# Performance work log

Hardware: AMD Instinct MI355X
Metric: run time of the kernel (lower is better)

## Reference

```python
import jax, jax.numpy as jnp
import numpy as np

D_MODEL = 256
N_HEADS = 8
HEAD_DIM = D_MODEL // N_HEADS


def setup_inputs() -> dict:
    key = jax.random.key(0)
    ks = jax.random.split(key, 10)
    B, L, D = 2, 2048, D_MODEL
    s = 1.0 / np.sqrt(D)
    inp = {
        "x": jax.random.normal(ks[0], (B, L, D), dtype=jnp.float32),
        "Wq": jax.random.normal(ks[1], (D, D), dtype=jnp.float32) * s,
        "bq": jnp.zeros((D,), jnp.float32),
        "Wk": jax.random.normal(ks[2], (D, D), dtype=jnp.float32) * s,
        "bk": jnp.zeros((D,), jnp.float32),
        "Wv": jax.random.normal(ks[3], (D, D), dtype=jnp.float32) * s,
        "bv": jnp.zeros((D,), jnp.float32),
        "u": jax.random.normal(ks[4], (N_HEADS, 1, 1), dtype=jnp.float32) * 0.1,
        "Wo": jax.random.normal(ks[5], (D, D), dtype=jnp.float32) * s,
        "bo": jnp.zeros((D,), jnp.float32),
    }
    return inp


def reference(x, Wq, bq, Wk, bk, Wv, bv, u, Wo, bo):
    B, L, D = x.shape
    H, hd = N_HEADS, HEAD_DIM

    def proj(W, b):  # torch Linear: x @ W.T + b -> [B,H,L,hd]
        return (x @ W.T + b).reshape(B, L, H, hd).transpose(0, 2, 1, 3)

    Q, K, V = proj(Wq, bq), proj(Wk, bk), proj(Wv, bv)

    scores = jnp.einsum("bhqd,bhkd->bhqk", Q, K) / np.sqrt(hd)
    attn_series = jax.nn.softmax(scores, axis=-1)  # [B,H,L,L]

    pos = jnp.arange(L, dtype=jnp.float32)
    dist = jnp.abs(pos[None, :] - pos[:, None])  # [L,L]
    # prior per head: exp(-d^2 / (2*(u^2+1e-6))), normalized over last dim
    prior = jnp.exp(-(dist[None] ** 2) / (2.0 * (u ** 2 + 1e-6)))  # [H,L,L]
    prior = prior / (prior.sum(axis=-1, keepdims=True) + 1e-6)

    discrepancy = jnp.abs(attn_series - prior[None]).mean(axis=(1, 2))  # [B,L]

    out = jnp.einsum("bhqk,bhkd->bhqd", attn_series, V)
    out = out.transpose(0, 2, 1, 3).reshape(B, L, D)
    out = out @ Wo.T + bo
    return out, discrepancy
```

## Files before the change

kernel.cpp:

```cpp
#include <hip/hip_runtime.h>
#include <hip/hip_bf16.h>
#include <math.h>

#define LSEQ 2048
#define DMODEL 256
#define NH 8
#define HD 32

typedef __attribute__((ext_vector_type(8))) short bf16x8;
typedef __attribute__((ext_vector_type(4))) float f32x4;

#define MFMA __builtin_amdgcn_mfma_f32_16x16x32_bf16

__device__ __forceinline__ short f2bf(float x) {
  __hip_bfloat16 h = __float2bfloat16(x);
  return __builtin_bit_cast(short, h);
}
__device__ __forceinline__ float bf2f(short s) {
  __hip_bfloat16 h = __builtin_bit_cast(__hip_bfloat16, s);
  return __bfloat162float(h);
}
__device__ __forceinline__ short bftrunc(float x) {
  return (short)(__builtin_bit_cast(unsigned int, x) >> 16);
}
__device__ __forceinline__ float fexp2(float x) {
#if __has_builtin(__builtin_amdgcn_exp2f)
  return __builtin_amdgcn_exp2f(x);
#else
  return __expf(x * 0.6931471805599453f);
#endif
}
__device__ __forceinline__ float flog2(float x) {
#if __has_builtin(__builtin_amdgcn_logf)
  return __builtin_amdgcn_logf(x);
#else
  return __logf(x) * 1.4426950408889634f;
#endif
}

__global__ __launch_bounds__(256) void aux_kernel(
    const float* __restrict__ Wq, const float* __restrict__ Wk,
    const float* __restrict__ Wv, const float* __restrict__ Wo,
    const float* __restrict__ u,
    short* __restrict__ Wh,
    short* __restrict__ Woh, short* __restrict__ Wol,
    float* __restrict__ Eb, float* __restrict__ Zb)
{
  __shared__ float Cs[LSEQ];
  __shared__ float part[256];
  const int tid = threadIdx.x;
  if (blockIdx.x < 256) {
    const int i4 = (blockIdx.x * 256 + tid) * 4;
    if (i4 < 196608) {
      int row = i4 >> 8, col = i4 & 255;
      const float* W = (row < 256) ? Wq : (row < 512) ? Wk : Wv;
      float4 v = *(const float4*)(W + (row & 255) * 256 + col);
      *(short4*)(Wh + i4) = make_short4(f2bf(v.x), f2bf(v.y), f2bf(v.z), f2bf(v.w));
    } else {
      int j = i4 - 196608;
      float4 v = *(const float4*)(Wo + j);
      short h0 = f2bf(v.x), h1 = f2bf(v.y), h2 = f2bf(v.z), h3 = f2bf(v.w);
      *(short4*)(Woh + j) = make_short4(h0, h1, h2, h3);
      *(short4*)(Wol + j) = make_short4(bftrunc(v.x - bf2f(h0)), bftrunc(v.y - bf2f(h1)),
                                        bftrunc(v.z - bf2f(h2)), bftrunc(v.w - bf2f(h3)));
    }
    return;
  }
  const int h = blockIdx.x - 256;
  const float uu = u[h];
  const float den = 2.0f * (uu * uu + 1e-6f);
  float e[8]; float run = 0.f;
  const int base = tid * 8;
#pragma unroll
  for (int j = 0; j < 8; ++j) {
    float d = (float)(base + j);
    e[j] = __expf(-(d * d) / den);
    run += e[j];
  }
  part[tid] = run;
  __syncthreads();
  for (int off = 1; off < 256; off <<= 1) {
    float v = (tid >= off) ? part[tid - off] : 0.f;
    __syncthreads();
    part[tid] += v;
    __syncthreads();
  }
  float c = part[tid] - run;
#pragma unroll
  for (int j = 0; j < 8; ++j) {
    c += e[j];
    Cs[base + j] = c;
    Eb[h * LSEQ + base + j] = e[j];
  }
  __syncthreads();
  const float E0 = Cs[0];
  for (int i = tid; i < LSEQ; i += 256) {
    float s = Cs[i] + Cs[LSEQ - 1 - i] - E0;
    Zb[h * LSEQ + i] = 1.0f / (s + 1e-6f);
  }
}

__global__ __launch_bounds__(256) void qkv_gemm(
    const float* __restrict__ x,
    const short* __restrict__ Bh,
    const float* __restrict__ bq, const float* __restrict__ bk,
    const float* __restrict__ bv,
    short* __restrict__ Qf, short* __restrict__ Kf, short* __restrict__ Vf)
{
  const int tid = threadIdx.x, w = tid >> 6, lane = tid & 63;
  const int l15 = lane & 15, q4 = lane >> 4;
  const int m0 = blockIdx.x * 64, n0 = blockIdx.y * 64;
  const int mrow = m0 + w * 16 + l15;
  f32x4 acc[4] = {{0,0,0,0},{0,0,0,0},{0,0,0,0},{0,0,0,0}};
  for (int k0 = 0; k0 < 256; k0 += 32) {
    const float* xp = &x[(size_t)mrow * 256 + k0 + q4 * 8];
    float4 a = *(const float4*)xp;
    float4 c = *(const float4*)(xp + 4);
    bf16x8 ah;
    ah[0] = f2bf(a.x); ah[1] = f2bf(a.y); ah[2] = f2bf(a.z); ah[3] = f2bf(a.w);
    ah[4] = f2bf(c.x); ah[5] = f2bf(c.y); ah[6] = f2bf(c.z); ah[7] = f2bf(c.w);
#pragma unroll
    for (int nt = 0; nt < 4; ++nt) {
      const size_t bi = (size_t)(n0 + nt * 16 + l15) * 256 + k0 + q4 * 8;
      bf16x8 bh = *(const bf16x8*)&Bh[bi];
      acc[nt] = MFMA(ah, bh, acc[nt], 0, 0, 0);
    }
  }
  const int type = n0 >> 8;
  const int n0l = n0 & 255;
  const float* bias = (type == 0) ? bq : (type == 1) ? bk : bv;
  const float qls = 0.25503489f;
#pragma unroll
  for (int nt = 0; nt < 4; ++nt) {
    const int col = n0l + nt * 16 + l15;
    const float bvv = bias[col];
    const int hh = col >> 5, dloc = col & 31;
#pragma unroll
    for (int r = 0; r < 4; ++r) {
      const int m = m0 + w * 16 + q4 * 4 + r;
      float v = acc[nt][r] + bvv;
      const int bb = m >> 11, mm = m & 2047, rr = mm & 15;
      if (type == 2) {
        const int kt128 = mm >> 7, low7 = mm & 127;
        const int wv = (low7 >> 4) & 3, ph = low7 >> 6;
        const int c = ph * 16 + rr;
        const size_t idx =
          ((((((size_t)bb * 8 + hh) * 16 + kt128) * 4 + wv) * 2 + (dloc >> 4)) * 64
           + (c >> 3) * 16 + (dloc & 15)) * 8 + (c & 7);
        Vf[idx] = f2bf(v);
      } else if (type == 0) {
        const int qblk = mm >> 5, rg = (mm >> 4) & 1;
        const size_t idx =
          (((((size_t)bb * 8 + hh) * 64 + qblk) * 2 + rg) * 64
           + (dloc >> 3) * 16 + rr) * 8 + (dloc & 7);
        Qf[idx] = f2bf(v * qls);
      } else {
        const int g = mm >> 4;
        const size_t idx =
          ((((size_t)bb * 8 + hh) * 128 + g) * 64
           + (dloc >> 3) * 16 + rr) * 8 + (dloc & 7);
        Kf[idx] = f2bf(v);
      }
    }
  }
}

__global__ __launch_bounds__(256) void out_gemm(
    const short* __restrict__ Ah, const short* __restrict__ Al,
    const short* __restrict__ Bh, const short* __restrict__ Bl,
    const float* __restrict__ bias, float* __restrict__ C)
{
  const int tid = threadIdx.x, w = tid >> 6, lane = tid & 63;
  const int l15 = lane & 15, q4 = lane >> 4;
  const int m0 = blockIdx.x * 64, n0 = blockIdx.y * 64;
  const int mrow = m0 + w * 16 + l15;
  f32x4 acc[4] = {{0,0,0,0},{0,0,0,0},{0,0,0,0},{0,0,0,0}};
  for (int k0 = 0; k0 < 256; k0 += 32) {
    bf16x8 ah = *(const bf16x8*)&Ah[(size_t)mrow * 256 + k0 + q4 * 8];
    bf16x8 al = *(const bf16x8*)&Al[(size_t)mrow * 256 + k0 + q4 * 8];
#pragma unroll
    for (int nt = 0; nt < 4; ++nt) {
      const size_t bi = (size_t)(n0 + nt * 16 + l15) * 256 + k0 + q4 * 8;
      bf16x8 bh = *(const bf16x8*)&Bh[bi];
      bf16x8 bl = *(const bf16x8*)&Bl[bi];
      acc[nt] = MFMA(ah, bh, acc[nt], 0, 0, 0);
      acc[nt] = MFMA(al, bh, acc[nt], 0, 0, 0);
      acc[nt] = MFMA(ah, bl, acc[nt], 0, 0, 0);
    }
  }
#pragma unroll
  for (int nt = 0; nt < 4; ++nt) {
    const int col = n0 + nt * 16 + l15;
    const float bvv = bias[col];
#pragma unroll
    for (int r = 0; r < 4; ++r) {
      const int m = m0 + w * 16 + q4 * 4 + r;
      C[(size_t)m * 256 + col] = acc[nt][r] + bvv;
    }
  }
}

__global__ __launch_bounds__(256, 8) void attn_kernel(
    const short* __restrict__ Qf, const short* __restrict__ Kf,
    const short* __restrict__ Vf,
    const float* __restrict__ Eb, const float* __restrict__ Zb,
    short* __restrict__ Ohb, short* __restrict__ Olb,
    short* __restrict__ Dp)
{
  __shared__ short Pt[4][16][40];
  __shared__ float Elds[192];
  __shared__ float lpart[4][16];
  __shared__ float izlds[16];

  const int tid = threadIdx.x, w = tid >> 6, lane = tid & 63;
  const int l15 = lane & 15, q4 = lane >> 4;
  const int flat = blockIdx.x + 128 * (blockIdx.y + 8 * blockIdx.z);
  const int slot = flat >> 3;
  const int g = (flat & 7) | ((slot >> 7) << 3);
  const int h = g & 7, b = g >> 3;
  const int qslot = slot & 127, q0 = qslot * 16;
  const int bh = b * NH + h;

  if (tid < 192) Elds[tid] = Eb[h * LSEQ + tid];
  if (tid < 16)  izlds[tid] = Zb[h * LSEQ + q0 + tid];

  const bf16x8* Qf8 = (const bf16x8*)Qf;
  const bf16x8* Kf8 = (const bf16x8*)Kf;
  const bf16x8* Vf8 = (const bf16x8*)Vf;

  bf16x8 qh = Qf8[((size_t)bh * 128 + qslot) * 64 + lane];
  __syncthreads();

  const size_t kfb = (size_t)bh * 128;
  const size_t vfb = (size_t)bh * 16;

  float lac[4] = {0.f, 0.f, 0.f, 0.f};
#pragma unroll 2
  for (int kt = 0; kt < LSEQ; kt += 128) {
    bf16x8 k0 = Kf8[(kfb + (kt >> 4) + w) * 64 + lane];
    bf16x8 k1 = Kf8[(kfb + (kt >> 4) + 4 + w) * 64 + lane];
    f32x4 s0 = {0.f, 0.f, 0.f, 0.f};
    s0 = MFMA(qh, k0, s0, 0, 0, 0);
    f32x4 s1 = {0.f, 0.f, 0.f, 0.f};
    s1 = MFMA(qh, k1, s1, 0, 0, 0);
#pragma unroll
    for (int r = 0; r < 4; ++r) lac[r] += fexp2(s0[r]) + fexp2(s1[r]);
  }
#pragma unroll
  for (int r = 0; r < 4; ++r) {
    float v = lac[r];
    v += __shfl_xor(v, 1); v += __shfl_xor(v, 2);
    v += __shfl_xor(v, 4); v += __shfl_xor(v, 8);
    lac[r] = v;
  }
  if (l15 == 0) {
#pragma unroll
    for (int r = 0; r < 4; ++r) lpart[w][q4 * 4 + r] = lac[r];
  }
  __syncthreads();
  f32x4 sinit;
#pragma unroll
  for (int r = 0; r < 4; ++r) {
    const int qi = q4 * 4 + r;
    sinit[r] = -flog2(lpart[0][qi] + lpart[1][qi] + lpart[2][qi] + lpart[3][qi]);
  }

  const size_t drow = (size_t)(g * 128 + qslot) * LSEQ;
  f32x4 oacc[2] = {{0,0,0,0},{0,0,0,0}};
#pragma unroll 2
  for (int kt = 0; kt < LSEQ; kt += 128) {
    bf16x8 kh0 = Kf8[(kfb + (kt >> 4) + w) * 64 + lane];
    bf16x8 kh1 = Kf8[(kfb + (kt >> 4) + 4 + w) * 64 + lane];
    bf16x8 vb0 = Vf8[(((vfb + (kt >> 7)) * 4 + w) * 2 + 0) * 64 + lane];
    bf16x8 vb1 = Vf8[(((vfb + (kt >> 7)) * 4 + w) * 2 + 1) * 64 + lane];
#pragma unroll
    for (int ph = 0; ph < 2; ++ph) {
      bf16x8 kbh = ph ? kh1 : kh0;
      const int c0 = kt + ph * 64 + w * 16;
      const int kg = c0 + l15;
      const int dd = c0 - q0;
      const bool near = (dd >= -96) && (dd <= 96);
      float dsum = 0.f;
      f32x4 s = sinit;
      s = MFMA(qh, kbh, s, 0, 0, 0);
#pragma unroll
      for (int r = 0; r < 4; ++r) {
        float p = fexp2(s[r]);
        Pt[w][q4 * 4 + r][ph * 16 + l15] = bftrunc(p);
        if (near) {
          int qrow = q0 + q4 * 4 + r;
          int dist = (qrow >= kg) ? (qrow - kg) : (kg - qrow);
          dsum += fabsf(p - Elds[dist] * izlds[q4 * 4 + r]);
        } else {
          dsum += p;
        }
      }
      dsum += __shfl_xor(dsum, 16);
      dsum += __shfl_xor(dsum, 32);
      if (q4 == 0) Dp[drow + kg] = f2bf(dsum);
    }
    bf16x8 pa = *(const bf16x8*)&Pt[w][l15][q4 * 8];
    oacc[0] = MFMA(pa, vb0, oacc[0], 0, 0, 0);
    oacc[1] = MFMA(pa, vb1, oacc[1], 0, 0, 0);
  }

  __syncthreads();
  float* Ored = (float*)&Pt[0][0][0];
#pragma unroll
  for (int dt = 0; dt < 2; ++dt) {
#pragma unroll
    for (int r = 0; r < 4; ++r)
      Ored[(w * 16 + q4 * 4 + r) * 17 + l15] = oacc[dt][r];
    __syncthreads();
    {
      const int q = tid >> 4, d = tid & 15;
      float v = Ored[q * 17 + d] + Ored[(16 + q) * 17 + d] +
                Ored[(32 + q) * 17 + d] + Ored[(48 + q) * 17 + d];
      const size_t oo = ((size_t)b * LSEQ + q0 + q) * DMODEL + h * HD + dt * 16 + d;
      short hi = f2bf(v);
      Ohb[oo] = hi;
      Olb[oo] = bftrunc(v - bf2f(hi));
    }
    __syncthreads();
  }
}

__global__ __launch_bounds__(256) void disc_reduce(
    const short* __restrict__ Dp, float* __restrict__ disc)
{
  __shared__ float red[8][33];
  const int tid = threadIdx.x;
  const int b = blockIdx.x >> 6;
  const int kb = (blockIdx.x & 63) * 32;
  const int k = kb + (tid & 31), sg = tid >> 5;
  float acc = 0.f;
  const short* base = Dp + ((size_t)b * 1024 + (size_t)sg * 128) * LSEQ + k;
#pragma unroll 4
  for (int i = 0; i < 128; ++i) acc += bf2f(base[(size_t)i * LSEQ]);
  red[sg][tid & 31] = acc;
  __syncthreads();
  if (tid < 32) {
    float v = 0.f;
#pragma unroll
    for (int s2 = 0; s2 < 8; ++s2) v += red[s2][tid];
    disc[b * LSEQ + kb + tid] = v * (1.0f / ((float)NH * (float)LSEQ));
  }
}

extern "C" void kernel_launch(void* const* d_in, const int* in_sizes, int n_in,
                              void* d_out, int out_size, void* d_ws, size_t ws_size,
                              hipStream_t stream)
{
  const float* x  = (const float*)d_in[0];
  const float* Wq = (const float*)d_in[1];
  const float* bq = (const float*)d_in[2];
  const float* Wk = (const float*)d_in[3];
  const float* bk = (const float*)d_in[4];
  const float* Wv = (const float*)d_in[5];
  const float* bv = (const float*)d_in[6];
  const float* u  = (const float*)d_in[7];
  const float* Wo = (const float*)d_in[8];
  const float* bo = (const float*)d_in[9];

  float* out  = (float*)d_out;
  float* disc = out + (size_t)2 * LSEQ * DMODEL;

  char* w8 = (char*)d_ws;
  const size_t MB = 1u << 20;
  short* Qfb = (short*)(w8);
  short* Kfb = (short*)(w8 + 2 * MB);
  short* Vfb = (short*)(w8 + 4 * MB);
  short* Ohb = (short*)(w8 + 6 * MB);
  short* Olb = (short*)(w8 + 8 * MB);
  short* Wh  = (short*)(w8 + 10 * MB);
  short* Woh = (short*)(w8 + 10 * MB + 393216);
  short* Wol = (short*)(w8 + 10 * MB + 524288);
  float* Eb  = (float*)(w8 + 11 * MB);
  float* Zb  = (float*)(w8 + 11 * MB + 65536);
  short* Dp  = (short*)(w8 + 12 * MB);

  aux_kernel<<<264, 256, 0, stream>>>(Wq, Wk, Wv, Wo, u, Wh, Woh, Wol, Eb, Zb);
  qkv_gemm<<<dim3(64, 12), 256, 0, stream>>>(x, Wh, bq, bk, bv, Qfb, Kfb, Vfb);
  attn_kernel<<<dim3(128, 8, 2), 256, 0, stream>>>(Qfb, Kfb, Vfb, Eb, Zb,
                                                   Ohb, Olb, Dp);
  disc_reduce<<<128, 256, 0, stream>>>(Dp, disc);
  out_gemm<<<dim3(64, 4), 256, 0, stream>>>(Ohb, Olb, Woh, Wol, bo, out);
}
```

Before: 156.7 us.

## Cache unnormalized probabilities in LDS, widen attention blocks, fuse tail kernels, pre-convert x

The attention kernel now keeps all 16x2048 unnormalized exp values in shared memory during the first pass and reuses them in the second pass. This drops the QK recompute and second exp, and normalization becomes a multiply by the reciprocal row sum. Blocks grow to 512 threads (8 waves) with a 64KB LDS tile, which lowers occupancy. The out GEMM and the discrepancy reduction are merged into one launch with narrower tiles for more blocks, and x is converted to bf16 once in the aux kernel rather than inside the QKV GEMM.

Result: slower. 165.4 us (+5.5%).

```diff
diff --git a/kernel.cpp b/kernel.cpp
--- a/kernel.cpp
+++ b/kernel.cpp
@@ -30,18 +30,13 @@
   return __expf(x * 0.6931471805599453f);
 #endif
 }
-__device__ __forceinline__ float flog2(float x) {
-#if __has_builtin(__builtin_amdgcn_logf)
-  return __builtin_amdgcn_logf(x);
-#else
-  return __logf(x) * 1.4426950408889634f;
-#endif
-}
 
 __global__ __launch_bounds__(256) void aux_kernel(
+    const float* __restrict__ x,
     const float* __restrict__ Wq, const float* __restrict__ Wk,
     const float* __restrict__ Wv, const float* __restrict__ Wo,
     const float* __restrict__ u,
+    short* __restrict__ xh,
     short* __restrict__ Wh,
     short* __restrict__ Woh, short* __restrict__ Wol,
     float* __restrict__ Eb, float* __restrict__ Zb)
@@ -49,8 +44,15 @@
   __shared__ float Cs[LSEQ];
   __shared__ float part[256];
   const int tid = threadIdx.x;
-  if (blockIdx.x < 256) {
+  if (blockIdx.x < 1024) {
     const int i4 = (blockIdx.x * 256 + tid) * 4;
+    float4 v = *(const float4*)(x + i4);
+    *(short4*)(xh + i4) = make_short4(f2bf(v.x), f2bf(v.y), f2bf(v.z), f2bf(v.w));
+    return;
+  }
+  const int bx = blockIdx.x - 1024;
+  if (bx < 256) {
+    const int i4 = (bx * 256 + tid) * 4;
     if (i4 < 196608) {
       int row = i4 >> 8, col = i4 & 255;
       const float* W = (row < 256) ? Wq : (row < 512) ? Wk : Wv;
@@ -66,7 +68,7 @@
     }
     return;
   }
-  const int h = blockIdx.x - 256;
+  const int h = bx - 256;
   const float uu = u[h];
   const float den = 2.0f * (uu * uu + 1e-6f);
   float e[8]; float run = 0.f;
@@ -101,7 +103,7 @@
 }
 
 __global__ __launch_bounds__(256) void qkv_gemm(
-    const float* __restrict__ x,
+    const short* __restrict__ xh,
     const short* __restrict__ Bh,
     const float* __restrict__ bq, const float* __restrict__ bk,
     const float* __restrict__ bv,
@@ -113,12 +115,7 @@
   const int mrow = m0 + w * 16 + l15;
   f32x4 acc[4] = {{0,0,0,0},{0,0,0,0},{0,0,0,0},{0,0,0,0}};
   for (int k0 = 0; k0 < 256; k0 += 32) {
-    const float* xp = &x[(size_t)mrow * 256 + k0 + q4 * 8];
-    float4 a = *(const float4*)xp;
-    float4 c = *(const float4*)(xp + 4);
-    bf16x8 ah;
-    ah[0] = f2bf(a.x); ah[1] = f2bf(a.y); ah[2] = f2bf(a.z); ah[3] = f2bf(a.w);
-    ah[4] = f2bf(c.x); ah[5] = f2bf(c.y); ah[6] = f2bf(c.z); ah[7] = f2bf(c.w);
+    bf16x8 ah = *(const bf16x8*)&xh[(size_t)mrow * 256 + k0 + q4 * 8];
 #pragma unroll
     for (int nt = 0; nt < 4; ++nt) {
       const size_t bi = (size_t)(n0 + nt * 16 + l15) * 256 + k0 + q4 * 8;
@@ -165,52 +162,18 @@
   }
 }
 
-__global__ __launch_bounds__(256) void out_gemm(
-    const short* __restrict__ Ah, const short* __restrict__ Al,
-    const short* __restrict__ Bh, const short* __restrict__ Bl,
-    const float* __restrict__ bias, float* __restrict__ C)
-{
-  const int tid = threadIdx.x, w = tid >> 6, lane = tid & 63;
-  const int l15 = lane & 15, q4 = lane >> 4;
-  const int m0 = blockIdx.x * 64, n0 = blockIdx.y * 64;
-  const int mrow = m0 + w * 16 + l15;
-  f32x4 acc[4] = {{0,0,0,0},{0,0,0,0},{0,0,0,0},{0,0,0,0}};
-  for (int k0 = 0; k0 < 256; k0 += 32) {
-    bf16x8 ah = *(const bf16x8*)&Ah[(size_t)mrow * 256 + k0 + q4 * 8];
-    bf16x8 al = *(const bf16x8*)&Al[(size_t)mrow * 256 + k0 + q4 * 8];
-#pragma unroll
-    for (int nt = 0; nt < 4; ++nt) {
-      const size_t bi = (size_t)(n0 + nt * 16 + l15) * 256 + k0 + q4 * 8;
-      bf16x8 bh = *(const bf16x8*)&Bh[bi];
-      bf16x8 bl = *(const bf16x8*)&Bl[bi];
-      acc[nt] = MFMA(ah, bh, acc[nt], 0, 0, 0);
-      acc[nt] = MFMA(al, bh, acc[nt], 0, 0, 0);
-      acc[nt] = MFMA(ah, bl, acc[nt], 0, 0, 0);
-    }
-  }
-#pragma unroll
-  for (int nt = 0; nt < 4; ++nt) {
-    const int col = n0 + nt * 16 + l15;
-    const float bvv = bias[col];
-#pragma unroll
-    for (int r = 0; r < 4; ++r) {
-      const int m = m0 + w * 16 + q4 * 4 + r;
-      C[(size_t)m * 256 + col] = acc[nt][r] + bvv;
-    }
-  }
-}
-
-__global__ __launch_bounds__(256, 8) void attn_kernel(
+__global__ __launch_bounds__(512, 4) void attn_kernel(
     const short* __restrict__ Qf, const short* __restrict__ Kf,
     const short* __restrict__ Vf,
     const float* __restrict__ Eb, const float* __restrict__ Zb,
     short* __restrict__ Ohb, short* __restrict__ Olb,
     short* __restrict__ Dp)
 {
-  __shared__ short Pt[4][16][40];
+  __shared__ short Pp[16 * 2048];
   __shared__ float Elds[192];
-  __shared__ float lpart[4][16];
-  __shared__ float izlds[16];
+  __shared__ float lpart[8][16];
+  __shared__ float lpn[16];
+  __shared__ float liz[16];
 
   const int tid = threadIdx.x, w = tid >> 6, lane = tid & 63;
   const int l15 = lane & 15, q4 = lane >> 4;
@@ -222,75 +185,84 @@
   const int bh = b * NH + h;
 
   if (tid < 192) Elds[tid] = Eb[h * LSEQ + tid];
-  if (tid < 16)  izlds[tid] = Zb[h * LSEQ + q0 + tid];
+  if (tid < 16)  liz[tid] = Zb[h * LSEQ + q0 + tid];
 
   const bf16x8* Qf8 = (const bf16x8*)Qf;
   const bf16x8* Kf8 = (const bf16x8*)Kf;
   const bf16x8* Vf8 = (const bf16x8*)Vf;
 
   bf16x8 qh = Qf8[((size_t)bh * 128 + qslot) * 64 + lane];
-  __syncthreads();
 
   const size_t kfb = (size_t)bh * 128;
   const size_t vfb = (size_t)bh * 16;
+  const int wv = w & 3, wh = w >> 2;
 
   float lac[4] = {0.f, 0.f, 0.f, 0.f};
 #pragma unroll 2
-  for (int kt = 0; kt < LSEQ; kt += 128) {
-    bf16x8 k0 = Kf8[(kfb + (kt >> 4) + w) * 64 + lane];
-    bf16x8 k1 = Kf8[(kfb + (kt >> 4) + 4 + w) * 64 + lane];
-    f32x4 s0 = {0.f, 0.f, 0.f, 0.f};
-    s0 = MFMA(qh, k0, s0, 0, 0, 0);
-    f32x4 s1 = {0.f, 0.f, 0.f, 0.f};
-    s1 = MFMA(qh, k1, s1, 0, 0, 0);
-#pragma unroll
-    for (int r = 0; r < 4; ++r) lac[r] += fexp2(s0[r]) + fexp2(s1[r]);
+  for (int it = 0; it < 8; ++it) {
+    const int g16 = it * 16 + wh * 8 + wv;
+    bf16x8 k0 = Kf8[(kfb + g16) * 64 + lane];
+    bf16x8 k1 = Kf8[(kfb + g16 + 4) * 64 + lane];
+    f32x4 s0 = {0.f,0.f,0.f,0.f}; s0 = MFMA(qh, k0, s0, 0, 0, 0);
+    f32x4 s1 = {0.f,0.f,0.f,0.f}; s1 = MFMA(qh, k1, s1, 0, 0, 0);
+    const int cc0 = it * 256 + w * 32 + l15;
+#pragma unroll
+    for (int r = 0; r < 4; ++r) {
+      const int row = q4 * 4 + r;
+      const int sw = (row & 7) << 3;
+      float p0 = fexp2(s0[r]);
+      float p1 = fexp2(s1[r]);
+      lac[r] += p0 + p1;
+      Pp[(row * 2048 + cc0) ^ sw]      = bftrunc(p0);
+      Pp[(row * 2048 + cc0 + 16) ^ sw] = bftrunc(p1);
+    }
   }
 #pragma unroll
   for (int r = 0; r < 4; ++r) {
     float v = lac[r];
     v += __shfl_xor(v, 1); v += __shfl_xor(v, 2);
     v += __shfl_xor(v, 4); v += __shfl_xor(v, 8);
-    lac[r] = v;
-  }
-  if (l15 == 0) {
-#pragma unroll
-    for (int r = 0; r < 4; ++r) lpart[w][q4 * 4 + r] = lac[r];
-  }
-  __syncthreads();
-  f32x4 sinit;
+    if (l15 == 0) lpart[w][q4 * 4 + r] = v;
+  }
+  __syncthreads();
+  if (tid < 16) {
+    float l = 0.f;
+#pragma unroll
+    for (int w8 = 0; w8 < 8; ++w8) l += lpart[w8][tid];
+    lpn[tid] = 1.0f / l;
+  }
+  __syncthreads();
+
+  float pn4[4], iz4[4];
 #pragma unroll
   for (int r = 0; r < 4; ++r) {
-    const int qi = q4 * 4 + r;
-    sinit[r] = -flog2(lpart[0][qi] + lpart[1][qi] + lpart[2][qi] + lpart[3][qi]);
+    pn4[r] = lpn[q4 * 4 + r];
+    iz4[r] = liz[q4 * 4 + r];
   }
 
   const size_t drow = (size_t)(g * 128 + qslot) * LSEQ;
   f32x4 oacc[2] = {{0,0,0,0},{0,0,0,0}};
 #pragma unroll 2
-  for (int kt = 0; kt < LSEQ; kt += 128) {
-    bf16x8 kh0 = Kf8[(kfb + (kt >> 4) + w) * 64 + lane];
-    bf16x8 kh1 = Kf8[(kfb + (kt >> 4) + 4 + w) * 64 + lane];
-    bf16x8 vb0 = Vf8[(((vfb + (kt >> 7)) * 4 + w) * 2 + 0) * 64 + lane];
-    bf16x8 vb1 = Vf8[(((vfb + (kt >> 7)) * 4 + w) * 2 + 1) * 64 + lane];
+  for (int it = 0; it < 8; ++it) {
+    const int kt128 = it * 2 + wh;
+    bf16x8 vb0 = Vf8[(((vfb + kt128) * 4 + wv) * 2 + 0) * 64 + lane];
+    bf16x8 vb1 = Vf8[(((vfb + kt128) * 4 + wv) * 2 + 1) * 64 + lane];
 #pragma unroll
     for (int ph = 0; ph < 2; ++ph) {
-      bf16x8 kbh = ph ? kh1 : kh0;
-      const int c0 = kt + ph * 64 + w * 16;
-      const int kg = c0 + l15;
-      const int dd = c0 - q0;
+      const int c0g = kt128 * 128 + ph * 64 + wv * 16;
+      const int kg = c0g + l15;
+      const int dd = c0g - q0;
       const bool near = (dd >= -96) && (dd <= 96);
+      const int ccd = it * 256 + w * 32 + ph * 16 + l15;
       float dsum = 0.f;
-      f32x4 s = sinit;
-      s = MFMA(qh, kbh, s, 0, 0, 0);
 #pragma unroll
       for (int r = 0; r < 4; ++r) {
-        float p = fexp2(s[r]);
-        Pt[w][q4 * 4 + r][ph * 16 + l15] = bftrunc(p);
+        const int row = q4 * 4 + r;
+        float p = bf2f(Pp[(row * 2048 + ccd) ^ ((row & 7) << 3)]) * pn4[r];
         if (near) {
-          int qrow = q0 + q4 * 4 + r;
+          int qrow = q0 + row;
           int dist = (qrow >= kg) ? (qrow - kg) : (kg - qrow);
-          dsum += fabsf(p - Elds[dist] * izlds[q4 * 4 + r]);
+          dsum += fabsf(p - Elds[dist] * iz4[r]);
         } else {
           dsum += p;
         }
@@ -299,23 +271,26 @@
       dsum += __shfl_xor(dsum, 32);
       if (q4 == 0) Dp[drow + kg] = f2bf(dsum);
     }
-    bf16x8 pa = *(const bf16x8*)&Pt[w][l15][q4 * 8];
+    const int cp = it * 256 + w * 32 + q4 * 8;
+    bf16x8 pa = *(const bf16x8*)&Pp[(l15 * 2048 + cp) ^ ((l15 & 7) << 3)];
     oacc[0] = MFMA(pa, vb0, oacc[0], 0, 0, 0);
     oacc[1] = MFMA(pa, vb1, oacc[1], 0, 0, 0);
   }
 
   __syncthreads();
-  float* Ored = (float*)&Pt[0][0][0];
+  float* Ored = (float*)Pp;
 #pragma unroll
   for (int dt = 0; dt < 2; ++dt) {
 #pragma unroll
     for (int r = 0; r < 4; ++r)
       Ored[(w * 16 + q4 * 4 + r) * 17 + l15] = oacc[dt][r];
     __syncthreads();
-    {
+    if (tid < 256) {
       const int q = tid >> 4, d = tid & 15;
-      float v = Ored[q * 17 + d] + Ored[(16 + q) * 17 + d] +
-                Ored[(32 + q) * 17 + d] + Ored[(48 + q) * 17 + d];
+      float v = 0.f;
+#pragma unroll
+      for (int w8 = 0; w8 < 8; ++w8) v += Ored[(w8 * 16 + q) * 17 + d];
+      v *= lpn[q];
       const size_t oo = ((size_t)b * LSEQ + q0 + q) * DMODEL + h * HD + dt * 16 + d;
       short hi = f2bf(v);
       Ohb[oo] = hi;
@@ -325,13 +300,47 @@
   }
 }
 
-__global__ __launch_bounds__(256) void disc_reduce(
+__global__ __launch_bounds__(256) void tail_kernel(
+    const short* __restrict__ Ah, const short* __restrict__ Al,
+    const short* __restrict__ Bh, const short* __restrict__ Bl,
+    const float* __restrict__ bias, float* __restrict__ C,
     const short* __restrict__ Dp, float* __restrict__ disc)
 {
   __shared__ float red[8][33];
   const int tid = threadIdx.x;
-  const int b = blockIdx.x >> 6;
-  const int kb = (blockIdx.x & 63) * 32;
+  if (blockIdx.x < 512) {
+    const int w = tid >> 6, lane = tid & 63;
+    const int l15 = lane & 15, q4 = lane >> 4;
+    const int m0 = (blockIdx.x & 63) * 64, n0 = (blockIdx.x >> 6) * 32;
+    const int mrow = m0 + w * 16 + l15;
+    f32x4 acc[2] = {{0,0,0,0},{0,0,0,0}};
+    for (int k0 = 0; k0 < 256; k0 += 32) {
+      bf16x8 ah = *(const bf16x8*)&Ah[(size_t)mrow * 256 + k0 + q4 * 8];
+      bf16x8 al = *(const bf16x8*)&Al[(size_t)mrow * 256 + k0 + q4 * 8];
+#pragma unroll
+      for (int nt = 0; nt < 2; ++nt) {
+        const size_t bi = (size_t)(n0 + nt * 16 + l15) * 256 + k0 + q4 * 8;
+        bf16x8 bh = *(const bf16x8*)&Bh[bi];
+        bf16x8 bl = *(const bf16x8*)&Bl[bi];
+        acc[nt] = MFMA(ah, bh, acc[nt], 0, 0, 0);
+        acc[nt] = MFMA(al, bh, acc[nt], 0, 0, 0);
+        acc[nt] = MFMA(ah, bl, acc[nt], 0, 0, 0);
+      }
+    }
+#pragma unroll
+    for (int nt = 0; nt < 2; ++nt) {
+      const int col = n0 + nt * 16 + l15;
+      const float bvv = bias[col];
+#pragma unroll
+      for (int r = 0; r < 4; ++r) {
+        const int m = m0 + w * 16 + q4 * 4 + r;
+        C[(size_t)m * 256 + col] = acc[nt][r] + bvv;
+      }
+    }
+    return;
+  }
+  const int bid = blockIdx.x - 512;
+  const int b = bid >> 6, kb = (bid & 63) * 32;
   const int k = kb + (tid & 31), sg = tid >> 5;
   float acc = 0.f;
   const short* base = Dp + ((size_t)b * 1024 + (size_t)sg * 128) * LSEQ + k;
@@ -377,12 +386,12 @@
   short* Wol = (short*)(w8 + 10 * MB + 524288);
   float* Eb  = (float*)(w8 + 11 * MB);
   float* Zb  = (float*)(w8 + 11 * MB + 65536);
-  short* Dp  = (short*)(w8 + 12 * MB);
-
-  aux_kernel<<<264, 256, 0, stream>>>(Wq, Wk, Wv, Wo, u, Wh, Woh, Wol, Eb, Zb);
-  qkv_gemm<<<dim3(64, 12), 256, 0, stream>>>(x, Wh, bq, bk, bv, Qfb, Kfb, Vfb);
-  attn_kernel<<<dim3(128, 8, 2), 256, 0, stream>>>(Qfb, Kfb, Vfb, Eb, Zb,
+  short* xh  = (short*)(w8 + 12 * MB);
+  short* Dp  = (short*)(w8 + 14 * MB);
+
+  aux_kernel<<<1288, 256, 0, stream>>>(x, Wq, Wk, Wv, Wo, u, xh, Wh, Woh, Wol, Eb, Zb);
+  qkv_gemm<<<dim3(64, 12), 256, 0, stream>>>(xh, Wh, bq, bk, bv, Qfb, Kfb, Vfb);
+  attn_kernel<<<dim3(128, 8, 2), 512, 0, stream>>>(Qfb, Kfb, Vfb, Eb, Zb,
                                                    Ohb, Olb, Dp);
-  disc_reduce<<<128, 256, 0, stream>>>(Dp, disc);
-  out_gemm<<<dim3(64, 4), 256, 0, stream>>>(Ohb, Olb, Woh, Wol, bo, out);
-}
+  tail_kernel<<<640, 256, 0, stream>>>(Ohb, Olb, Woh, Wol, bo, out, Dp, disc);
+}
```
